# Optimization experiments

Measured on AMD Instinct MI355X. Metric: run time of the kernel, lower is better.

The kernel has to match this reference:

```python
import jax, jax.numpy as jnp
import numpy as np

N_HEAD = 8
D_MODEL = 512
D_HEAD = D_MODEL // N_HEAD
SCALE = 1.0 / D_HEAD ** 0.5
CLIP = 10.0


def setup_inputs() -> dict:
    key = jax.random.key(0)
    k1, k2, k3 = jax.random.split(key, 3)
    q = jax.random.normal(k1, (1, 32, D_MODEL), dtype=jnp.float32)
    k = jax.random.normal(k2, (8192, 32, D_MODEL), dtype=jnp.float32)
    v = jax.random.normal(k3, (8192, 32, D_MODEL), dtype=jnp.float32)
    return {"q": q, "k": k, "v": v}


def reference(q, k, v):
    qlen, bsz, _ = q.shape
    klen = k.shape[0]
    # split heads: (len, B, H) -> (len, B, nh, d)
    qh = q.reshape(qlen, bsz, N_HEAD, D_HEAD)
    kh = k.reshape(klen, bsz, N_HEAD, D_HEAD)
    vh = v.reshape(klen, bsz, N_HEAD, D_HEAD)
    # scores (i, j, B, nh)
    score = jnp.einsum('ibnd,jbnd->ijbn', qh, kh) * SCALE
    score = CLIP * jnp.tanh(score)
    weight = jax.nn.softmax(score, axis=1)
    out = jnp.einsum('ijbn,jbnd->ibnd', weight, vh)
    return out.reshape(qlen, bsz, N_HEAD * D_HEAD)
```

## Files before the change

### kernel.cpp

```cpp
#include <hip/hip_runtime.h>


#define N_PAIR    256
#define DH        64
#define KLEN      8192
#define SPLITS    8
#define ROWSTRIDE 16384
#define SCALE_F   0.125f
#define CLIP_F    10.0f

__global__ __launch_bounds__(256) void attn_partial(
    const float* __restrict__ q, const float* __restrict__ k,
    const float* __restrict__ v, float* __restrict__ part_num,
    float* __restrict__ part_den)
{
    const int p    = blockIdx.x & (N_PAIR - 1);
    const int s    = blockIdx.x >> 8;
    const int tid  = threadIdx.x;
    const int lane = tid & 63;
    const int w    = tid >> 6;
    const int dd   = lane & 15;
    const int jj   = lane >> 4;

    const int base = p * DH;
    const float4 qv = *(const float4*)(q + base + dd * 4);

    float4 acc = make_float4(0.f, 0.f, 0.f, 0.f);
    float  den = 0.f;

    const int jbase = s * (KLEN / SPLITS);
    const int niter = (KLEN / SPLITS) / 16;

    #pragma unroll 4
    for (int it = 0; it < niter; ++it) {
        const int j = jbase + it * 16 + w * 4 + jj;
        const size_t off = (size_t)j * ROWSTRIDE + base + dd * 4;
        const float4 kv = *(const float4*)(k + off);
        const float4 vv = *(const float4*)(v + off);

        float pd = kv.x * qv.x + kv.y * qv.y + kv.z * qv.z + kv.w * qv.w;
        pd += __shfl_xor(pd, 1);
        pd += __shfl_xor(pd, 2);
        pd += __shfl_xor(pd, 4);
        pd += __shfl_xor(pd, 8);

        const float x  = pd * SCALE_F;
        const float e2 = __expf(2.f * x);
        const float th = 1.f - 2.f / (e2 + 1.f);
        const float wg = __expf(CLIP_F * th);

        acc.x += wg * vv.x;
        acc.y += wg * vv.y;
        acc.z += wg * vv.z;
        acc.w += wg * vv.w;
        den   += wg;
    }

    acc.x += __shfl_xor(acc.x, 16); acc.x += __shfl_xor(acc.x, 32);
    acc.y += __shfl_xor(acc.y, 16); acc.y += __shfl_xor(acc.y, 32);
    acc.z += __shfl_xor(acc.z, 16); acc.z += __shfl_xor(acc.z, 32);
    acc.w += __shfl_xor(acc.w, 16); acc.w += __shfl_xor(acc.w, 32);
    den   += __shfl_xor(den, 16);   den   += __shfl_xor(den, 32);

    __shared__ float lacc[4][DH];
    __shared__ float lden[4];
    if (lane < 16) {
        lacc[w][dd * 4 + 0] = acc.x;
        lacc[w][dd * 4 + 1] = acc.y;
        lacc[w][dd * 4 + 2] = acc.z;
        lacc[w][dd * 4 + 3] = acc.w;
        if (lane == 0) lden[w] = den;
    }
    __syncthreads();
    if (tid < DH) {
        const float num = lacc[0][tid] + lacc[1][tid] + lacc[2][tid] + lacc[3][tid];
        const float dn  = lden[0] + lden[1] + lden[2] + lden[3];
        part_num[(size_t)blockIdx.x * DH + tid] = num;
        if (tid == 0) part_den[blockIdx.x] = dn;
    }
}

__global__ __launch_bounds__(64) void attn_reduce(
    const float* __restrict__ part_num, const float* __restrict__ part_den,
    float* __restrict__ out)
{
    const int p = blockIdx.x;
    const int d = threadIdx.x;
    float num = 0.f, den = 0.f;
    #pragma unroll
    for (int s = 0; s < SPLITS; ++s) {
        const int slot = s * N_PAIR + p;
        num += part_num[(size_t)slot * DH + d];
        den += part_den[slot];
    }
    out[p * DH + d] = num / den;
}

extern "C" void kernel_launch(void* const* d_in, const int* in_sizes, int n_in,
                              void* d_out, int out_size, void* d_ws, size_t ws_size,
                              hipStream_t stream)
{
    const float* q = (const float*)d_in[0];
    const float* k = (const float*)d_in[1];
    const float* v = (const float*)d_in[2];
    float* out = (float*)d_out;

    float* part_num = (float*)d_ws;
    float* part_den = part_num + (size_t)SPLITS * N_PAIR * DH;

    attn_partial<<<dim3(SPLITS * N_PAIR), dim3(256), 0, stream>>>(
        q, k, v, part_num, part_den);
    attn_reduce<<<dim3(N_PAIR), dim3(64), 0, stream>>>(part_num, part_den, out);
}
```

Measured before the change: 982.8 us.

## Map each block to a batch row covering all heads for contiguous K/V reads

```diff
diff --git a/kernel.cpp b/kernel.cpp
--- a/kernel.cpp
+++ b/kernel.cpp
@@ -1,11 +1,13 @@
 #include <hip/hip_runtime.h>
 
 
-#define N_PAIR    256
+#define BATCH     32
+#define NH        8
 #define DH        64
+#define DMODEL    512
 #define KLEN      8192
-#define SPLITS    8
-#define ROWSTRIDE 16384
+#define SPLITS    64
+#define ROWS_PB   (KLEN / SPLITS)
 #define SCALE_F   0.125f
 #define CLIP_F    10.0f
 
@@ -14,86 +16,87 @@
     const float* __restrict__ v, float* __restrict__ part_num,
     float* __restrict__ part_den)
 {
-    const int p    = blockIdx.x & (N_PAIR - 1);
-    const int s    = blockIdx.x >> 8;
+    const int b    = blockIdx.x & (BATCH - 1);
+    const int s    = blockIdx.x >> 5;
     const int tid  = threadIdx.x;
+    const int w    = tid >> 6;
     const int lane = tid & 63;
-    const int w    = tid >> 6;
-    const int dd   = lane & 15;
-    const int jj   = lane >> 4;
+    const int n    = lane >> 3;
+    const int dsl  = (lane & 7) * 8;
 
-    const int base = p * DH;
-    const float4 qv = *(const float4*)(q + base + dd * 4);
+    const float* qp = q + b * DMODEL + n * DH + dsl;
+    float4 q0 = *(const float4*)(qp);
+    float4 q1 = *(const float4*)(qp + 4);
+    q0.x *= SCALE_F; q0.y *= SCALE_F; q0.z *= SCALE_F; q0.w *= SCALE_F;
+    q1.x *= SCALE_F; q1.y *= SCALE_F; q1.z *= SCALE_F; q1.w *= SCALE_F;
 
-    float4 acc = make_float4(0.f, 0.f, 0.f, 0.f);
+    const size_t base = (size_t)(s * ROWS_PB + w) * (BATCH * DMODEL)
+                      + b * DMODEL + n * DH + dsl;
+    const float* kp = k + base;
+    const float* vp = v + base;
+    const size_t step = (size_t)4 * BATCH * DMODEL;
+
+    float4 a0 = make_float4(0.f, 0.f, 0.f, 0.f);
+    float4 a1 = make_float4(0.f, 0.f, 0.f, 0.f);
     float  den = 0.f;
 
-    const int jbase = s * (KLEN / SPLITS);
-    const int niter = (KLEN / SPLITS) / 16;
+    #pragma unroll 2
+    for (int it = 0; it < ROWS_PB / 4; ++it) {
+        const float4 k0 = *(const float4*)(kp);
+        const float4 k1 = *(const float4*)(kp + 4);
+        const float4 v0 = *(const float4*)(vp);
+        const float4 v1 = *(const float4*)(vp + 4);
+        kp += step; vp += step;
 
-    #pragma unroll 4
-    for (int it = 0; it < niter; ++it) {
-        const int j = jbase + it * 16 + w * 4 + jj;
-        const size_t off = (size_t)j * ROWSTRIDE + base + dd * 4;
-        const float4 kv = *(const float4*)(k + off);
-        const float4 vv = *(const float4*)(v + off);
-
-        float pd = kv.x * qv.x + kv.y * qv.y + kv.z * qv.z + kv.w * qv.w;
+        float pd = k0.x * q0.x + k0.y * q0.y + k0.z * q0.z + k0.w * q0.w
+                 + k1.x * q1.x + k1.y * q1.y + k1.z * q1.z + k1.w * q1.w;
         pd += __shfl_xor(pd, 1);
         pd += __shfl_xor(pd, 2);
         pd += __shfl_xor(pd, 4);
-        pd += __shfl_xor(pd, 8);
 
-        const float x  = pd * SCALE_F;
-        const float e2 = __expf(2.f * x);
+        const float e2 = __expf(2.f * pd);
         const float th = 1.f - 2.f / (e2 + 1.f);
         const float wg = __expf(CLIP_F * th);
 
-        acc.x += wg * vv.x;
-        acc.y += wg * vv.y;
-        acc.z += wg * vv.z;
-        acc.w += wg * vv.w;
-        den   += wg;
+        a0.x += wg * v0.x; a0.y += wg * v0.y; a0.z += wg * v0.z; a0.w += wg * v0.w;
+        a1.x += wg * v1.x; a1.y += wg * v1.y; a1.z += wg * v1.z; a1.w += wg * v1.w;
+        den  += wg;
     }
 
-    acc.x += __shfl_xor(acc.x, 16); acc.x += __shfl_xor(acc.x, 32);
-    acc.y += __shfl_xor(acc.y, 16); acc.y += __shfl_xor(acc.y, 32);
-    acc.z += __shfl_xor(acc.z, 16); acc.z += __shfl_xor(acc.z, 32);
-    acc.w += __shfl_xor(acc.w, 16); acc.w += __shfl_xor(acc.w, 32);
-    den   += __shfl_xor(den, 16);   den   += __shfl_xor(den, 32);
+    __shared__ float lacc[4][DMODEL];
+    __shared__ float lden[4][NH];
+    ((float4*)&lacc[w][lane * 8])[0] = a0;
+    ((float4*)&lacc[w][lane * 8])[1] = a1;
+    if ((lane & 7) == 0) lden[w][n] = den;
+    __syncthreads();
 
-    __shared__ float lacc[4][DH];
-    __shared__ float lden[4];
-    if (lane < 16) {
-        lacc[w][dd * 4 + 0] = acc.x;
-        lacc[w][dd * 4 + 1] = acc.y;
-        lacc[w][dd * 4 + 2] = acc.z;
-        lacc[w][dd * 4 + 3] = acc.w;
-        if (lane == 0) lden[w] = den;
+    #pragma unroll
+    for (int r = 0; r < 2; ++r) {
+        const int c = tid + r * 256;
+        const float num = lacc[0][c] + lacc[1][c] + lacc[2][c] + lacc[3][c];
+        part_num[(size_t)blockIdx.x * DMODEL + c] = num;
     }
-    __syncthreads();
-    if (tid < DH) {
-        const float num = lacc[0][tid] + lacc[1][tid] + lacc[2][tid] + lacc[3][tid];
-        const float dn  = lden[0] + lden[1] + lden[2] + lden[3];
-        part_num[(size_t)blockIdx.x * DH + tid] = num;
-        if (tid == 0) part_den[blockIdx.x] = dn;
+    if (tid < NH) {
+        part_den[blockIdx.x * NH + tid] =
+            lden[0][tid] + lden[1][tid] + lden[2][tid] + lden[3][tid];
     }
 }
 
-__global__ __launch_bounds__(64) void attn_reduce(
+__global__ __launch_bounds__(512) void attn_reduce(
     const float* __restrict__ part_num, const float* __restrict__ part_den,
     float* __restrict__ out)
 {
-    const int p = blockIdx.x;
-    const int d = threadIdx.x;
+    const int b = blockIdx.x;
+    const int c = threadIdx.x;
+    const int n = c >> 6;
     float num = 0.f, den = 0.f;
-    #pragma unroll
+    #pragma unroll 8
     for (int s = 0; s < SPLITS; ++s) {
-        const int slot = s * N_PAIR + p;
-        num += part_num[(size_t)slot * DH + d];
-        den += part_den[slot];
+        const int slot = s * BATCH + b;
+        num += part_num[(size_t)slot * DMODEL + c];
+        den += part_den[slot * NH + n];
     }
-    out[p * DH + d] = num / den;
+    out[b * DMODEL + c] = num / den;
 }
 
 extern "C" void kernel_launch(void* const* d_in, const int* in_sizes, int n_in,
@@ -106,9 +109,9 @@
     float* out = (float*)d_out;
 
     float* part_num = (float*)d_ws;
-    float* part_den = part_num + (size_t)SPLITS * N_PAIR * DH;
+    float* part_den = part_num + (size_t)SPLITS * BATCH * DMODEL;
 
-    attn_partial<<<dim3(SPLITS * N_PAIR), dim3(256), 0, stream>>>(
+    attn_partial<<<dim3(SPLITS * BATCH), dim3(256), 0, stream>>>(
         q, k, v, part_num, part_den);
-    attn_reduce<<<dim3(N_PAIR), dim3(64), 0, stream>>>(part_num, part_den, out);
+    attn_reduce<<<dim3(BATCH), dim3(512), 0, stream>>>(part_num, part_den, out);
 }
```

Result: no change. 1.001 ms (+1.9%).
